# Kernel tuning notes

Measured on AMD Instinct MI355X. Metric: run time of the kernel, lower is better.

The kernel has to match this reference:

```python
import math
import jax, jax.numpy as jnp
import numpy as np

N_HEADS = 16
D_EMBED = 1024
D_HEAD = D_EMBED // N_HEADS
B, S = 4, 2048


def setup_inputs() -> dict:
    key = jax.random.key(0)
    k1, k2, k3, k4, k5 = jax.random.split(key, 5)
    scale_in = 1.0 / math.sqrt(D_EMBED)
    return {
        "x": jax.random.normal(k1, (B, S, D_EMBED), dtype=jnp.float32),
        "w_in": jax.random.normal(k2, (3 * D_EMBED, D_EMBED), dtype=jnp.float32) * scale_in,
        "b_in": jax.random.normal(k3, (3 * D_EMBED,), dtype=jnp.float32) * 0.02,
        "w_out": jax.random.normal(k4, (D_EMBED, D_EMBED), dtype=jnp.float32) * scale_in,
        "b_out": jax.random.normal(k5, (D_EMBED,), dtype=jnp.float32) * 0.02,
        "causal_mask": 1,
    }


def reference(x, w_in, b_in, w_out, b_out, causal_mask):
    Bn, Sn, D = x.shape
    # fused QKV projection (torch Linear: x @ W.T + b)
    qkv = x @ w_in.T + b_in                       # (B, S, 3D)
    q, k, v = jnp.split(qkv, 3, axis=-1)
    def to_heads(t):
        return t.reshape(Bn, Sn, N_HEADS, D_HEAD).transpose(0, 2, 1, 3)  # (B,H,S,dh)
    q, k, v = to_heads(q), to_heads(k), to_heads(v)
    # manual scaled dot-product attention, full (B,H,S,S) scores
    scores = jnp.einsum("bhqd,bhkd->bhqk", q, k)
    if causal_mask:
        tri = jnp.triu(jnp.ones((Sn, Sn), dtype=bool), k=1)
        scores = jnp.where(tri, -jnp.inf, scores)
    scores = scores / math.sqrt(D_HEAD)
    weights = jax.nn.softmax(scores, axis=-1)
    out = jnp.einsum("bhqk,bhkd->bhqd", weights, v)  # (B,H,S,dh)
    out = out.transpose(0, 2, 1, 3).reshape(Bn, Sn, D)
    return out @ w_out.T + b_out
```

## Files before the change

kernel.cpp:

```cpp
#include <hip/hip_runtime.h>

typedef __bf16 bf16x8 __attribute__((ext_vector_type(8)));
typedef float  f32x4  __attribute__((ext_vector_type(4)));
typedef unsigned int uint;

__device__ inline unsigned short f2bf(float f) {
  union { float f; unsigned int u; } v; v.f = f;
  unsigned int u = v.u;
  unsigned int r = u + 0x7FFF + ((u >> 16) & 1);
  return (unsigned short)(r >> 16);
}

__device__ inline uint pack_bf16_rhu(float a, float b) {
  uint ua = __builtin_bit_cast(uint, a) + 0x8000u;
  uint ub = __builtin_bit_cast(uint, b) + 0x8000u;
  return __builtin_amdgcn_perm(ub, ua, 0x07060302u);
}

__device__ inline void load_lds16(const unsigned short* g, unsigned short* l) {
  __builtin_amdgcn_global_load_lds(
      (const __attribute__((address_space(1))) uint*)(g),
      (__attribute__((address_space(3))) uint*)(l), 16, 0, 0);
}

__device__ inline void cvt4(const float* in, unsigned short* out) {
  float4 f = *reinterpret_cast<const float4*>(in);
  ushort4 o;
  o.x = f2bf(f.x); o.y = f2bf(f.y); o.z = f2bf(f.z); o.w = f2bf(f.w);
  *reinterpret_cast<ushort4*>(out) = o;
}

__global__ void cvt_all(const float* __restrict__ x, const float* __restrict__ w_in,
                        const float* __restrict__ w_out,
                        unsigned short* __restrict__ x_bf,
                        unsigned short* __restrict__ w_in_bf,
                        unsigned short* __restrict__ w_out_bf) {
  const int n1 = 8192 * 1024, n2 = 3072 * 1024;
  int i = (blockIdx.x * blockDim.x + threadIdx.x) * 4;
  if (i < n1)            cvt4(x + i, x_bf + i);
  else if (i < n1 + n2)  cvt4(w_in + (i - n1), w_in_bf + (i - n1));
  else                   cvt4(w_out + (i - n1 - n2), w_out_bf + (i - n1 - n2));
}

template<bool OUT_BF16, bool VSPLIT>
__global__ __launch_bounds__(256) void gemm_bt128(
    const unsigned short* __restrict__ A,
    const unsigned short* __restrict__ B,
    const float* __restrict__ bias,
    void* __restrict__ Cout,
    unsigned short* __restrict__ vt,
    int M, int N, int K, int ldc, float scale, int ncut)
{
  __shared__ __attribute__((aligned(16))) unsigned short As[128 * 64];
  __shared__ __attribute__((aligned(16))) unsigned short Bs[128 * 64];

  const int t    = threadIdx.x;
  const int wave = t >> 6, lane = t & 63;
  const int l16  = lane & 15, quad = lane >> 4;
  const int wr = wave >> 1, wc = wave & 1;
  const int m0 = blockIdx.y * 128, n0 = blockIdx.x * 128;
  const int l8 = l16 & 7;

  f32x4 acc[4][4] = {};

  for (int k0 = 0; k0 < K; k0 += 64) {
#pragma unroll
    for (int i = 0; i < 4; ++i) {
      int chunk = i * 256 + t;
      int row = chunk >> 3, cb = chunk & 7;
      int gcb = cb ^ (row & 7);
      load_lds16(A + (size_t)(m0 + row) * K + k0 + gcb * 8, As + chunk * 8);
    }
#pragma unroll
    for (int i = 0; i < 4; ++i) {
      int chunk = i * 256 + t;
      int row = chunk >> 3, cb = chunk & 7;
      int gcb = cb ^ (row & 7);
      load_lds16(B + (size_t)(n0 + row) * K + k0 + gcb * 8, Bs + chunk * 8);
    }
    __syncthreads();
#pragma unroll
    for (int ks = 0; ks < 2; ++ks) {
      bf16x8 af[4], bfr[4];
#pragma unroll
      for (int mt = 0; mt < 4; ++mt)
        af[mt] = *(const bf16x8*)(As + (wr * 64 + mt * 16 + l16) * 64 +
                                  (((ks * 4 + quad) ^ l8) << 3));
#pragma unroll
      for (int nt = 0; nt < 4; ++nt)
        bfr[nt] = *(const bf16x8*)(Bs + (wc * 64 + nt * 16 + l16) * 64 +
                                   (((ks * 4 + quad) ^ l8) << 3));
#pragma unroll
      for (int mt = 0; mt < 4; ++mt)
#pragma unroll
        for (int nt = 0; nt < 4; ++nt)
          acc[mt][nt] = __builtin_amdgcn_mfma_f32_16x16x32_bf16(af[mt], bfr[nt], acc[mt][nt], 0, 0, 0);
    }
    __syncthreads();
  }

#pragma unroll
  for (int nt = 0; nt < 4; ++nt) {
    int col = n0 + wc * 64 + nt * 16 + l16;
    float bv = bias[col];
    float mlt = (col < ncut) ? scale : 1.0f;
#pragma unroll
    for (int mt = 0; mt < 4; ++mt) {
      int row0 = m0 + wr * 64 + mt * 16 + quad * 4;
      float v0 = (acc[mt][nt][0] + bv) * mlt;
      float v1 = (acc[mt][nt][1] + bv) * mlt;
      float v2 = (acc[mt][nt][2] + bv) * mlt;
      float v3 = (acc[mt][nt][3] + bv) * mlt;
      if (VSPLIT && col >= 2048) {
        int d = col - 2048, h = d >> 6, dd = d & 63;
        int bb = row0 >> 11, s = row0 & 2047;
        uint2 w;
        w.x = pack_bf16_rhu(v0, v1);
        w.y = pack_bf16_rhu(v2, v3);
        *(uint2*)(vt + ((size_t)((bb * 16 + h) * 64 + dd) * 2048 + s)) = w;
      } else {
#pragma unroll
        for (int r = 0; r < 4; ++r) {
          float v = (r == 0) ? v0 : (r == 1) ? v1 : (r == 2) ? v2 : v3;
          if (OUT_BF16)
            ((unsigned short*)Cout)[(size_t)(row0 + r) * ldc + col] = f2bf(v);
          else
            ((float*)Cout)[(size_t)(row0 + r) * ldc + col] = v;
        }
      }
    }
  }
}

__global__ __launch_bounds__(256) void attn(
    const unsigned short* __restrict__ qkv2,
    const unsigned short* __restrict__ vt,
    unsigned short* __restrict__ y,
    const int* __restrict__ flag)
{
  __shared__ __attribute__((aligned(16))) unsigned short Qs[128][72];
  __shared__ __attribute__((aligned(16))) unsigned short Ks[64][72];
  __shared__ __attribute__((aligned(16))) unsigned short VtF[64 * 64];

  const int t    = threadIdx.x;
  const int wave = t >> 6, lane = t & 63;
  const int l16  = lane & 15, quad = lane >> 4;
  const int idx = blockIdx.x;
  const int bh  = idx & 63;
  const int g   = idx >> 6, ph = g >> 2, gr = g & 3;
  const int qt  = (ph == 0) ? (15 - gr) : (ph == 1) ? gr : (ph == 2) ? (11 - gr) : (4 + gr);
  const int b = bh >> 4, h = bh & 15;
  const int causal = flag[0];
  const int q0 = qt * 128;

  const unsigned short* Qg = qkv2 + (size_t)b * 2048 * 2048 + h * 64;
  const unsigned short* Kg = Qg + 1024;
  const unsigned short* Vtg = vt + (size_t)bh * 64 * 2048;

  {
    int r = t >> 1, c0 = (t & 1) * 32;
    const unsigned short* src = Qg + (size_t)(q0 + r) * 2048 + c0;
#pragma unroll
    for (int i = 0; i < 4; ++i)
      *(uint4*)&Qs[r][c0 + i * 8] = *(const uint4*)(src + i * 8);
  }
  __syncthreads();
  bf16x8 qf[2][2];
#pragma unroll
  for (int su = 0; su < 2; ++su) {
    qf[su][0] = *(const bf16x8*)&Qs[wave * 32 + su * 16 + l16][quad * 8];
    qf[su][1] = *(const bf16x8*)&Qs[wave * 32 + su * 16 + l16][32 + quad * 8];
  }
  __syncthreads();
  unsigned short (*Ps)[72] = Qs;

  f32x4 ot[2][4] = {};
  float l_lane[2] = {0.f, 0.f};
  const int qg0 = q0 + wave * 32 + l16;
  const int jmax = causal ? (2 * qt + 1) : 31;

  const int kr = t >> 2, kc = (t & 3) * 16;
  const int vd = t >> 2, vb = t & 3;
  const int vpos0 = ((vb     + vd) & 7) << 3;
  const int vpos1 = ((vb + 4 + vd) & 7) << 3;
  const unsigned short* vrow = Vtg + (size_t)vd * 2048;

  uint4 kreg0, kreg1, vreg0, vreg1;
  {
    const unsigned short* src = Kg + (size_t)kr * 2048 + kc;
    kreg0 = *(const uint4*)src;
    kreg1 = *(const uint4*)(src + 8);
    vreg0 = *(const uint4*)(vrow + vb * 8);
    vreg1 = *(const uint4*)(vrow + vb * 8 + 32);
  }

  for (int j = 0; j <= jmax; ++j) {
    *(uint4*)&Ks[kr][kc]     = kreg0;
    *(uint4*)&Ks[kr][kc + 8] = kreg1;
    *(uint4*)(VtF + vd * 64 + vpos0) = vreg0;
    *(uint4*)(VtF + vd * 64 + vpos1) = vreg1;
    __syncthreads();

    if (j < jmax) {
      const int kvn = (j + 1) * 64;
      const unsigned short* src = Kg + (size_t)(kvn + kr) * 2048 + kc;
      kreg0 = *(const uint4*)src;
      kreg1 = *(const uint4*)(src + 8);
      vreg0 = *(const uint4*)(vrow + kvn + vb * 8);
      vreg1 = *(const uint4*)(vrow + kvn + vb * 8 + 32);
    }

    f32x4 st[2][4] = {};
#pragma unroll
    for (int ks = 0; ks < 2; ++ks) {
#pragma unroll
      for (int mt = 0; mt < 4; ++mt) {
        bf16x8 kf = *(const bf16x8*)&Ks[mt * 16 + l16][ks * 32 + quad * 8];
        st[0][mt] = __builtin_amdgcn_mfma_f32_16x16x32_bf16(kf, qf[0][ks], st[0][mt], 0, 0, 0);
        st[1][mt] = __builtin_amdgcn_mfma_f32_16x16x32_bf16(kf, qf[1][ks], st[1][mt], 0, 0, 0);
      }
    }

    const bool diag = (causal != 0) && (j >= 2 * qt);
    const int kv0 = j * 64;
#pragma unroll
    for (int su = 0; su < 2; ++su) {
      const int qg = qg0 + su * 16;
#pragma unroll
      for (int mt = 0; mt < 4; ++mt) {
        float p[4];
#pragma unroll
        for (int r = 0; r < 4; ++r) {
          float pv = __builtin_amdgcn_exp2f(st[su][mt][r]);
          if (diag) {
            int kv = kv0 + mt * 16 + quad * 4 + r;
            if (kv > qg) pv = 0.f;
          }
          p[r] = pv;
        }
        l_lane[su] += (p[0] + p[1]) + (p[2] + p[3]);
        uint2 w;
        w.x = pack_bf16_rhu(p[0], p[1]);
        w.y = pack_bf16_rhu(p[2], p[3]);
        *(uint2*)&Ps[wave * 32 + su * 16 + l16][mt * 16 + quad * 4] = w;
      }
    }
    __threadfence_block();

#pragma unroll
    for (int ks = 0; ks < 2; ++ks) {
      bf16x8 pf0 = *(const bf16x8*)&Ps[wave * 32 + l16][ks * 32 + quad * 8];
      bf16x8 pf1 = *(const bf16x8*)&Ps[wave * 32 + 16 + l16][ks * 32 + quad * 8];
#pragma unroll
      for (int mt = 0; mt < 4; ++mt) {
        int pos = ((ks * 4 + quad + l16) & 7) << 3;
        bf16x8 vf = *(const bf16x8*)(VtF + (mt * 16 + l16) * 64 + pos);
        ot[0][mt] = __builtin_amdgcn_mfma_f32_16x16x32_bf16(vf, pf0, ot[0][mt], 0, 0, 0);
        ot[1][mt] = __builtin_amdgcn_mfma_f32_16x16x32_bf16(vf, pf1, ot[1][mt], 0, 0, 0);
      }
    }
    __syncthreads();
  }

#pragma unroll
  for (int su = 0; su < 2; ++su) {
    float l = l_lane[su];
    l += __shfl_xor(l, 16);
    l += __shfl_xor(l, 32);
    float inv = 1.f / l;
#pragma unroll
    for (int mt = 0; mt < 4; ++mt) {
      uint2 w;
      w.x = pack_bf16_rhu(ot[su][mt][0] * inv, ot[su][mt][1] * inv);
      w.y = pack_bf16_rhu(ot[su][mt][2] * inv, ot[su][mt][3] * inv);
      *(uint2*)&Ps[wave * 32 + su * 16 + l16][mt * 16 + quad * 4] = w;
    }
  }
  __syncthreads();
  {
    int r = t >> 1, c0 = (t & 1) * 32;
    size_t base = ((size_t)b * 2048 + q0 + r) * 1024 + h * 64 + c0;
#pragma unroll
    for (int i = 0; i < 4; ++i)
      *(uint4*)(y + base + i * 8) = *(const uint4*)&Ps[r][c0 + i * 8];
  }
}

extern "C" void kernel_launch(void* const* d_in, const int* in_sizes, int n_in,
                              void* d_out, int out_size, void* d_ws, size_t ws_size,
                              hipStream_t stream) {
  const float* x     = (const float*)d_in[0];
  const float* w_in  = (const float*)d_in[1];
  const float* b_in  = (const float*)d_in[2];
  const float* w_out = (const float*)d_in[3];
  const float* b_out = (const float*)d_in[4];
  const int*   cmask = (const int*)d_in[5];

  char* ws = (char*)d_ws;
  unsigned short* x_bf     = (unsigned short*)(ws);
  unsigned short* w_in_bf  = (unsigned short*)(ws + 16777216);
  unsigned short* w_out_bf = (unsigned short*)(ws + 23068672);
  unsigned short* qkv2_bf  = (unsigned short*)(ws + 25165824);
  unsigned short* vt_bf    = (unsigned short*)(ws + 58720256);
  unsigned short* y_bf     = (unsigned short*)(ws + 75497472);

  const int ntot = (8192 + 3072 + 1024) * 1024;
  cvt_all<<<dim3(ntot / 4 / 256), 256, 0, stream>>>(x, w_in, w_out, x_bf, w_in_bf, w_out_bf);

  gemm_bt128<true, true><<<dim3(24, 64), 256, 0, stream>>>(
      x_bf, w_in_bf, b_in, qkv2_bf, vt_bf, 8192, 3072, 1024, 2048,
      0.18033688011112042f, 1024);

  attn<<<dim3(1024), 256, 0, stream>>>(qkv2_bf, vt_bf, y_bf, cmask);

  gemm_bt128<false, false><<<dim3(8, 64), 256, 0, stream>>>(
      y_bf, w_out_bf, b_out, d_out, nullptr, 8192, 1024, 1024, 1024, 1.0f, 0);
}
```

Measured before the change: 259.9 us.

## Shrink attention query tile to 64 rows with XOR-swizzled LDS layout

The attention kernel now gives each block 64 query rows instead of 128, so each wave handles 16 rows and the grid doubles to 2048 blocks. Block scheduling becomes a simple descending order rather than the paired-phase mapping. Padded LDS arrays are replaced by XOR-swizzled 64x64 tiles for Q, K, V and P to avoid bank conflicts without padding. The aim is more parallelism, finer causal work granularity and fewer registers per thread, at the cost of reloading each K/V tile twice as often per query row.

```diff
diff --git a/kernel.cpp b/kernel.cpp
--- a/kernel.cpp
+++ b/kernel.cpp
@@ -138,56 +138,53 @@
     unsigned short* __restrict__ y,
     const int* __restrict__ flag)
 {
-  __shared__ __attribute__((aligned(16))) unsigned short Qs[128][72];
-  __shared__ __attribute__((aligned(16))) unsigned short Ks[64][72];
+  __shared__ __attribute__((aligned(16))) unsigned short Qs[64 * 64];
+  __shared__ __attribute__((aligned(16))) unsigned short Ks[64 * 64];
   __shared__ __attribute__((aligned(16))) unsigned short VtF[64 * 64];
 
   const int t    = threadIdx.x;
   const int wave = t >> 6, lane = t & 63;
   const int l16  = lane & 15, quad = lane >> 4;
+  const int l8   = l16 & 7;
   const int idx = blockIdx.x;
   const int bh  = idx & 63;
-  const int g   = idx >> 6, ph = g >> 2, gr = g & 3;
-  const int qt  = (ph == 0) ? (15 - gr) : (ph == 1) ? gr : (ph == 2) ? (11 - gr) : (4 + gr);
+  const int qt  = 31 - (idx >> 6);
   const int b = bh >> 4, h = bh & 15;
   const int causal = flag[0];
-  const int q0 = qt * 128;
+  const int q0 = qt * 64;
 
   const unsigned short* Qg = qkv2 + (size_t)b * 2048 * 2048 + h * 64;
   const unsigned short* Kg = Qg + 1024;
   const unsigned short* Vtg = vt + (size_t)bh * 64 * 2048;
 
+  const int sr = t >> 2, sg = (t & 3) * 2;
+  const int slot0 = sr * 64 + (((sg    ) ^ (sr & 7)) << 3);
+  const int slot1 = sr * 64 + (((sg + 1) ^ (sr & 7)) << 3);
+  const int vb = t & 3;
+  const int vslot0 = sr * 64 + ((( vb     ) ^ (sr & 7)) << 3);
+  const int vslot1 = sr * 64 + (((vb + 4) ^ (sr & 7)) << 3);
+  const unsigned short* vrow = Vtg + (size_t)sr * 2048;
+
   {
-    int r = t >> 1, c0 = (t & 1) * 32;
-    const unsigned short* src = Qg + (size_t)(q0 + r) * 2048 + c0;
-#pragma unroll
-    for (int i = 0; i < 4; ++i)
-      *(uint4*)&Qs[r][c0 + i * 8] = *(const uint4*)(src + i * 8);
+    const unsigned short* src = Qg + (size_t)(q0 + sr) * 2048 + sg * 8;
+    *(uint4*)(Qs + slot0) = *(const uint4*)src;
+    *(uint4*)(Qs + slot1) = *(const uint4*)(src + 8);
   }
   __syncthreads();
-  bf16x8 qf[2][2];
-#pragma unroll
-  for (int su = 0; su < 2; ++su) {
-    qf[su][0] = *(const bf16x8*)&Qs[wave * 32 + su * 16 + l16][quad * 8];
-    qf[su][1] = *(const bf16x8*)&Qs[wave * 32 + su * 16 + l16][32 + quad * 8];
-  }
+  bf16x8 qf[2];
+  qf[0] = *(const bf16x8*)(Qs + (wave * 16 + l16) * 64 + (((0 * 4 + quad) ^ l8) << 3));
+  qf[1] = *(const bf16x8*)(Qs + (wave * 16 + l16) * 64 + (((1 * 4 + quad) ^ l8) << 3));
   __syncthreads();
-  unsigned short (*Ps)[72] = Qs;
-
-  f32x4 ot[2][4] = {};
-  float l_lane[2] = {0.f, 0.f};
-  const int qg0 = q0 + wave * 32 + l16;
-  const int jmax = causal ? (2 * qt + 1) : 31;
-
-  const int kr = t >> 2, kc = (t & 3) * 16;
-  const int vd = t >> 2, vb = t & 3;
-  const int vpos0 = ((vb     + vd) & 7) << 3;
-  const int vpos1 = ((vb + 4 + vd) & 7) << 3;
-  const unsigned short* vrow = Vtg + (size_t)vd * 2048;
+  unsigned short* Ps = Qs;
+
+  f32x4 ot[4] = {};
+  float l_lane = 0.f;
+  const int q_glob = q0 + wave * 16 + l16;
+  const int jmax = causal ? qt : 31;
 
   uint4 kreg0, kreg1, vreg0, vreg1;
   {
-    const unsigned short* src = Kg + (size_t)kr * 2048 + kc;
+    const unsigned short* src = Kg + (size_t)sr * 2048 + sg * 8;
     kreg0 = *(const uint4*)src;
     kreg1 = *(const uint4*)(src + 8);
     vreg0 = *(const uint4*)(vrow + vb * 8);
@@ -195,94 +192,83 @@
   }
 
   for (int j = 0; j <= jmax; ++j) {
-    *(uint4*)&Ks[kr][kc]     = kreg0;
-    *(uint4*)&Ks[kr][kc + 8] = kreg1;
-    *(uint4*)(VtF + vd * 64 + vpos0) = vreg0;
-    *(uint4*)(VtF + vd * 64 + vpos1) = vreg1;
+    *(uint4*)(Ks + slot0)   = kreg0;
+    *(uint4*)(Ks + slot1)   = kreg1;
+    *(uint4*)(VtF + vslot0) = vreg0;
+    *(uint4*)(VtF + vslot1) = vreg1;
     __syncthreads();
 
     if (j < jmax) {
       const int kvn = (j + 1) * 64;
-      const unsigned short* src = Kg + (size_t)(kvn + kr) * 2048 + kc;
+      const unsigned short* src = Kg + (size_t)(kvn + sr) * 2048 + sg * 8;
       kreg0 = *(const uint4*)src;
       kreg1 = *(const uint4*)(src + 8);
       vreg0 = *(const uint4*)(vrow + kvn + vb * 8);
       vreg1 = *(const uint4*)(vrow + kvn + vb * 8 + 32);
     }
 
-    f32x4 st[2][4] = {};
+    f32x4 st[4] = {};
 #pragma unroll
     for (int ks = 0; ks < 2; ++ks) {
 #pragma unroll
       for (int mt = 0; mt < 4; ++mt) {
-        bf16x8 kf = *(const bf16x8*)&Ks[mt * 16 + l16][ks * 32 + quad * 8];
-        st[0][mt] = __builtin_amdgcn_mfma_f32_16x16x32_bf16(kf, qf[0][ks], st[0][mt], 0, 0, 0);
-        st[1][mt] = __builtin_amdgcn_mfma_f32_16x16x32_bf16(kf, qf[1][ks], st[1][mt], 0, 0, 0);
+        bf16x8 kf = *(const bf16x8*)(Ks + (mt * 16 + l16) * 64 + (((ks * 4 + quad) ^ l8) << 3));
+        st[mt] = __builtin_amdgcn_mfma_f32_16x16x32_bf16(kf, qf[ks], st[mt], 0, 0, 0);
       }
     }
 
-    const bool diag = (causal != 0) && (j >= 2 * qt);
+    const bool diag = (causal != 0) && (j == qt);
     const int kv0 = j * 64;
 #pragma unroll
-    for (int su = 0; su < 2; ++su) {
-      const int qg = qg0 + su * 16;
+    for (int mt = 0; mt < 4; ++mt) {
+      float p[4];
+#pragma unroll
+      for (int r = 0; r < 4; ++r) {
+        float pv = __builtin_amdgcn_exp2f(st[mt][r]);
+        if (diag) {
+          int kv = kv0 + mt * 16 + quad * 4 + r;
+          if (kv > q_glob) pv = 0.f;
+        }
+        p[r] = pv;
+      }
+      l_lane += (p[0] + p[1]) + (p[2] + p[3]);
+      uint2 w;
+      w.x = pack_bf16_rhu(p[0], p[1]);
+      w.y = pack_bf16_rhu(p[2], p[3]);
+      *(uint2*)(Ps + (wave * 16 + l16) * 64 +
+                ((((mt * 2 + (quad >> 1)) ^ l8) << 3) + (quad & 1) * 4)) = w;
+    }
+    __threadfence_block();
+
+#pragma unroll
+    for (int ks = 0; ks < 2; ++ks) {
+      bf16x8 pf = *(const bf16x8*)(Ps + (wave * 16 + l16) * 64 + (((ks * 4 + quad) ^ l8) << 3));
 #pragma unroll
       for (int mt = 0; mt < 4; ++mt) {
-        float p[4];
-#pragma unroll
-        for (int r = 0; r < 4; ++r) {
-          float pv = __builtin_amdgcn_exp2f(st[su][mt][r]);
-          if (diag) {
-            int kv = kv0 + mt * 16 + quad * 4 + r;
-            if (kv > qg) pv = 0.f;
-          }
-          p[r] = pv;
-        }
-        l_lane[su] += (p[0] + p[1]) + (p[2] + p[3]);
-        uint2 w;
-        w.x = pack_bf16_rhu(p[0], p[1]);
-        w.y = pack_bf16_rhu(p[2], p[3]);
-        *(uint2*)&Ps[wave * 32 + su * 16 + l16][mt * 16 + quad * 4] = w;
+        bf16x8 vf = *(const bf16x8*)(VtF + (mt * 16 + l16) * 64 + (((ks * 4 + quad) ^ l8) << 3));
+        ot[mt] = __builtin_amdgcn_mfma_f32_16x16x32_bf16(vf, pf, ot[mt], 0, 0, 0);
       }
     }
-    __threadfence_block();
-
-#pragma unroll
-    for (int ks = 0; ks < 2; ++ks) {
-      bf16x8 pf0 = *(const bf16x8*)&Ps[wave * 32 + l16][ks * 32 + quad * 8];
-      bf16x8 pf1 = *(const bf16x8*)&Ps[wave * 32 + 16 + l16][ks * 32 + quad * 8];
-#pragma unroll
-      for (int mt = 0; mt < 4; ++mt) {
-        int pos = ((ks * 4 + quad + l16) & 7) << 3;
-        bf16x8 vf = *(const bf16x8*)(VtF + (mt * 16 + l16) * 64 + pos);
-        ot[0][mt] = __builtin_amdgcn_mfma_f32_16x16x32_bf16(vf, pf0, ot[0][mt], 0, 0, 0);
-        ot[1][mt] = __builtin_amdgcn_mfma_f32_16x16x32_bf16(vf, pf1, ot[1][mt], 0, 0, 0);
-      }
-    }
     __syncthreads();
   }
 
-#pragma unroll
-  for (int su = 0; su < 2; ++su) {
-    float l = l_lane[su];
-    l += __shfl_xor(l, 16);
-    l += __shfl_xor(l, 32);
-    float inv = 1.f / l;
-#pragma unroll
-    for (int mt = 0; mt < 4; ++mt) {
-      uint2 w;
-      w.x = pack_bf16_rhu(ot[su][mt][0] * inv, ot[su][mt][1] * inv);
-      w.y = pack_bf16_rhu(ot[su][mt][2] * inv, ot[su][mt][3] * inv);
-      *(uint2*)&Ps[wave * 32 + su * 16 + l16][mt * 16 + quad * 4] = w;
-    }
+  l_lane += __shfl_xor(l_lane, 16);
+  l_lane += __shfl_xor(l_lane, 32);
+  float inv = 1.f / l_lane;
+
+#pragma unroll
+  for (int mt = 0; mt < 4; ++mt) {
+    uint2 w;
+    w.x = pack_bf16_rhu(ot[mt][0] * inv, ot[mt][1] * inv);
+    w.y = pack_bf16_rhu(ot[mt][2] * inv, ot[mt][3] * inv);
+    *(uint2*)(Ps + (wave * 16 + l16) * 64 +
+              ((((mt * 2 + (quad >> 1)) ^ l8) << 3) + (quad & 1) * 4)) = w;
   }
   __syncthreads();
   {
-    int r = t >> 1, c0 = (t & 1) * 32;
-    size_t base = ((size_t)b * 2048 + q0 + r) * 1024 + h * 64 + c0;
-#pragma unroll
-    for (int i = 0; i < 4; ++i)
-      *(uint4*)(y + base + i * 8) = *(const uint4*)&Ps[r][c0 + i * 8];
+    size_t base = ((size_t)b * 2048 + q0 + sr) * 1024 + h * 64 + sg * 8;
+    *(uint4*)(y + base)     = *(const uint4*)(Ps + slot0);
+    *(uint4*)(y + base + 8) = *(const uint4*)(Ps + slot1);
   }
 }
 
@@ -311,7 +297,7 @@
       x_bf, w_in_bf, b_in, qkv2_bf, vt_bf, 8192, 3072, 1024, 2048,
       0.18033688011112042f, 1024);
 
-  attn<<<dim3(1024), 256, 0, stream>>>(qkv2_bf, vt_bf, y_bf, cmask);
+  attn<<<dim3(2048), 256, 0, stream>>>(qkv2_bf, vt_bf, y_bf, cmask);
 
   gemm_bt128<false, false><<<dim3(8, 64), 256, 0, stream>>>(
       y_bf, w_out_bf, b_out, d_out, nullptr, 8192, 1024, 1024, 1024, 1.0f, 0);
```

Result: faster. 246.7 us (-5.1%).
